# Optimization experiments

Measured on AMD Instinct MI355X. Metric: run time of the kernel, lower is better.

The kernel has to match this reference:

```python
import jax, jax.numpy as jnp
import numpy as np
from jax import lax

N = 5000          # num atoms
E = 4             # num edge types
DIM_H = 128
VOCAB = 100       # num_atoms_vocab; embedding table has VOCAB+1 rows
T = 4             # max_time_steps


def setup_inputs() -> dict:
    key = jax.random.key(0)
    k1, k2, k3, k4 = jax.random.split(key, 4)
    atom_arr = jax.random.randint(k1, (N,), 0, VOCAB, dtype=jnp.int64 if jax.config.read('jax_enable_x64') else jnp.int32)
    adjs = jax.random.randint(k2, (E, N, N), 0, 2, dtype=jnp.int32)
    # learned parameters
    embedding = jax.random.normal(k3, (VOCAB + 1, DIM_H), dtype=jnp.float32) * 0.05
    limit = float(np.sqrt(6.0 / (DIM_H + DIM_H)))  # glorot uniform
    H_edges = jax.random.uniform(k4, (E, DIM_H, DIM_H), minval=-limit, maxval=limit, dtype=jnp.float32)
    return {
        "atom_arr": atom_arr,
        "adjs": adjs,
        "max_time_steps": T,
        "embedding": embedding,
        "H_edges": H_edges,
    }


def reference(atom_arr, adjs, max_time_steps, embedding, H_edges):
    # h_v^0 = embedding lookup, [N, H]
    h0 = embedding[atom_arr]
    # adjacency mask as float, [E, N, N]
    A = (adjs == 1).astype(h0.dtype)

    def step(h, _):
        # original: for each node v, edge type e: H_e @ sum_{u: adj[e,v,u]==1} h_u
        agg = jnp.einsum('evu,uh->evh', A, h)          # neighbor sum per edge type
        msg = jnp.einsum('eij,evj->vi', H_edges, agg)  # edge-type transform + sum over e
        h_new = jax.nn.sigmoid(h + msg)
        return h_new, h_new

    _, h_all = lax.scan(step, h0, None, length=max_time_steps)
    return h_all  # [T, N, H]
```

## Files before the change

### kernel.cpp

```cpp
#include <hip/hip_runtime.h>

#define NROW 5000
#define NPAD 5120
#define KPAD 5120
#define KW   80
#define KC   80
#define KZ   4
#define KCQ  20
#define HDIM 128
#define FXS  4194304.0f
#define PART ((size_t)4 * NROW * HDIM)

typedef _Float16 f16x8 __attribute__((ext_vector_type(8)));
typedef float f32x16 __attribute__((ext_vector_type(16)));

__device__ __forceinline__ unsigned short f2h_int(int v) {
    union { _Float16 h; unsigned short u; } c;
    c.h = (_Float16)(float)v;
    return c.u;
}
__device__ __forceinline__ void fx_digits(float h, unsigned short& d1, unsigned short& d0) {
    int q = (int)rintf(h * FXS);
    d1 = f2h_int(q >> 11);
    d0 = f2h_int(q & 2047);
}

__device__ __forceinline__ size_t ht_idx(int pl, int kc, int i, int kin) {
    return (((size_t)pl * KC + kc) * HDIM + i) * 64 + kin;
}

__global__ __launch_bounds__(256) void prep_atom_kernel(const unsigned int* __restrict__ atomw,
                                                        int* __restrict__ atomIdx) {
    __shared__ int s_is64;
    if (threadIdx.x == 0) {
        bool all0 = true, anynz = false;
        for (int j = 0; j < 64; ++j) {
            unsigned lo = atomw[2 * j], hi = atomw[2 * j + 1];
            all0 = all0 && (hi == 0u);
            anynz = anynz || (lo != 0u);
        }
        s_is64 = (all0 && anynz) ? 1 : 0;
    }
    __syncthreads();
    int v = blockIdx.x * 256 + threadIdx.x;
    if (v < NROW) atomIdx[v] = s_is64 ? (int)atomw[2 * v] : (int)atomw[v];
}

__global__ __launch_bounds__(256) void prep_pack_kernel(const int* __restrict__ adjs,
                                                        unsigned long long* __restrict__ packed) {
    const int er = blockIdx.x;
    const int e = er / NPAD;
    const int r = er - e * NPAD;
    const int wave = threadIdx.x >> 6;
    const int lane = threadIdx.x & 63;
    const int* rowp = adjs + ((size_t)e * NROW + r) * NROW;
    unsigned long long* outp = packed + ((size_t)e * NPAD + r) * KW;
    const bool rok = (r < NROW);
    for (int c = wave; c < KW; c += 4) {
        int u = c * 64 + lane;
        int val = (rok && u < NROW) ? rowp[u] : 0;
        unsigned long long m = __ballot(val == 1);
        if (lane == 0) outp[c] = m;
    }
}

__global__ __launch_bounds__(256) void prep_h0T_kernel(const int* __restrict__ atomIdx,
                                                       const float* __restrict__ emb,
                                                       unsigned short* __restrict__ hTt) {
    const int i = blockIdx.y;
    const int v = blockIdx.x * 256 + threadIdx.x;
    float val = 0.f;
    if (v < NROW) val = emb[(size_t)atomIdx[v] * HDIM + i];
    unsigned short d1, d0;
    fx_digits(val, d1, d0);
    hTt[ht_idx(0, v >> 6, i, v & 63)] = d1;
    hTt[ht_idx(1, v >> 6, i, v & 63)] = d0;
}

__global__ __launch_bounds__(256) void prep_h0f_kernel(const int* __restrict__ atomIdx,
                                                       const float* __restrict__ emb,
                                                       float* __restrict__ h) {
    int idx = blockIdx.x * 256 + threadIdx.x;
    int v = idx >> 7, i = idx & 127;
    h[idx] = emb[(size_t)atomIdx[v] * HDIM + i];
}

__global__ __launch_bounds__(256) void prep_Ht_kernel(const float* __restrict__ H,
                                                      float* __restrict__ Htr) {
    int idx = blockIdx.x * 256 + threadIdx.x;
    int e = idx >> 14;
    int j = (idx >> 7) & 127;
    int i = idx & 127;
    Htr[idx] = H[((size_t)e * HDIM + i) * HDIM + j];
}

__global__ __launch_bounds__(256, 2) void gemm1_kernel(const uint2* __restrict__ packed2,
                                                       const unsigned short* __restrict__ hTt,
                                                       float* __restrict__ agg) {
    const int m0 = blockIdx.x * 128;
    const int e = blockIdx.y;
    const int kz = blockIdx.z;
    const int tid = threadIdx.x;
    const int lane = tid & 63;
    const int wave = tid >> 6;
    const int l31 = lane & 31;
    const int l1 = lane >> 5;
    const int sh2 = l1 * 8;
    const int cb = wave * 32;
    const int col = cb + l31;

    f32x16 acc[2][4];
#pragma unroll
    for (int pl = 0; pl < 2; ++pl)
#pragma unroll
        for (int mt = 0; mt < 4; ++mt) acc[pl][mt] = (f32x16)(0.f);

    const uint2* ap[4];
#pragma unroll
    for (int mt = 0; mt < 4; ++mt)
        ap[mt] = packed2 + ((size_t)e * NPAD + (m0 + mt * 32 + l31)) * KW;

    const _Float16* bbase = (const _Float16*)hTt;
    const int kc0 = kz * KCQ;
    const _Float16* bp[2];
#pragma unroll
    for (int pl = 0; pl < 2; ++pl)
        bp[pl] = bbase + (((size_t)pl * KC + kc0) * HDIM + col) * 64 + sh2;

    for (int kc = kc0; kc < kc0 + KCQ; ++kc) {
        uint2 aw[4];
#pragma unroll
        for (int mt = 0; mt < 4; ++mt) aw[mt] = ap[mt][kc];
        const size_t coff = (size_t)(kc - kc0) * (HDIM * 64);

        f16x8 bf[2][4];
#pragma unroll
        for (int pl = 0; pl < 2; ++pl)
#pragma unroll
            for (int kk = 0; kk < 4; ++kk)
                bf[pl][kk] = *(const f16x8*)(bp[pl] + coff + kk * 16);

#pragma unroll
        for (int kk = 0; kk < 4; ++kk) {
#pragma unroll
            for (int mt = 0; mt < 4; ++mt) {
                unsigned int w = (kk < 2) ? aw[mt].x : aw[mt].y;
                unsigned int b = (w >> ((kk & 1) * 16 + sh2)) & 0xFFu;
                unsigned int y = b | (b << 15);
                union { unsigned int u[4]; f16x8 h; } A;
#pragma unroll
                for (int q = 0; q < 4; ++q)
                    A.u[q] = ((y >> (2 * q)) & 0x00010001u) * 0x3C00u;
#pragma unroll
                for (int pl = 0; pl < 2; ++pl)
                    acc[pl][mt] = __builtin_amdgcn_mfma_f32_32x32x16_f16(
                        A.h, bf[pl][kk], acc[pl][mt], 0, 0, 0);
            }
        }
    }

    float* aggz = agg + (size_t)kz * PART;
#pragma unroll
    for (int mt = 0; mt < 4; ++mt)
#pragma unroll
        for (int reg = 0; reg < 16; ++reg) {
            int row = (reg & 3) + 8 * (reg >> 2) + 4 * l1;
            int v = m0 + mt * 32 + row;
            if (v < NROW) {
                double d = (double)acc[0][mt][reg] * 2048.0 + (double)acc[1][mt][reg];
                aggz[((size_t)e * NROW + v) * HDIM + col] = (float)(d * (1.0 / 4194304.0));
            }
        }
}

__global__ __launch_bounds__(256) void gemm2_kernel(const float* __restrict__ agg,
                                                    const float* __restrict__ Htr,
                                                    float* __restrict__ h,
                                                    float* __restrict__ outp,
                                                    unsigned short* __restrict__ hTt) {
    __shared__ float aggs[16][512];
    __shared__ unsigned short hs[2][128][16];
    const int v0 = blockIdx.x * 16;
    const int tid = threadIdx.x;

#pragma unroll
    for (int it = 0; it < 8; ++it) {
        int idx = it * 256 + tid;
        int vv = idx >> 7;
        int ej = (idx & 127) * 4;
        int e = ej >> 7, j = ej & 127;
        int v = v0 + vv;
        float4 val = make_float4(0.f, 0.f, 0.f, 0.f);
        if (v < NROW) {
            size_t o = ((size_t)e * NROW + v) * HDIM + j;
            float4 a0 = *(const float4*)&agg[o];
            float4 a1 = *(const float4*)&agg[PART + o];
            float4 a2 = *(const float4*)&agg[2 * PART + o];
            float4 a3 = *(const float4*)&agg[3 * PART + o];
            val = make_float4((a0.x + a1.x) + (a2.x + a3.x), (a0.y + a1.y) + (a2.y + a3.y),
                              (a0.z + a1.z) + (a2.z + a3.z), (a0.w + a1.w) + (a2.w + a3.w));
        }
        *(float4*)&aggs[vv][ej] = val;
    }
    __syncthreads();

    const int i = tid & 127;
    const int vg = tid >> 7;
    float m4[8][4];
#pragma unroll
    for (int vv = 0; vv < 8; ++vv)
#pragma unroll
        for (int k = 0; k < 4; ++k) m4[vv][k] = 0.f;

    for (int c = 0; c < 512; c += 4) {
        float w0 = Htr[(size_t)(c + 0) * HDIM + i];
        float w1 = Htr[(size_t)(c + 1) * HDIM + i];
        float w2 = Htr[(size_t)(c + 2) * HDIM + i];
        float w3 = Htr[(size_t)(c + 3) * HDIM + i];
#pragma unroll
        for (int vv = 0; vv < 8; ++vv) {
            const float4 a = *(const float4*)&aggs[vg * 8 + vv][c];
            m4[vv][0] += a.x * w0;
            m4[vv][1] += a.y * w1;
            m4[vv][2] += a.z * w2;
            m4[vv][3] += a.w * w3;
        }
    }

#pragma unroll
    for (int vv = 0; vv < 8; ++vv) {
        int v = v0 + vg * 8 + vv;
        unsigned short d1 = 0, d0 = 0;
        if (v < NROW) {
            size_t o = (size_t)v * HDIM + i;
            float msg = (m4[vv][0] + m4[vv][1]) + (m4[vv][2] + m4[vv][3]);
            float x = h[o] + msg;
            float s = 1.0f / (1.0f + expf(-x));
            outp[o] = s;
            h[o] = s;
            fx_digits(s, d1, d0);
        }
        hs[0][i][vg * 8 + vv] = d1;
        hs[1][i][vg * 8 + vv] = d0;
    }
    __syncthreads();
    if (tid < 128) {
#pragma unroll
        for (int pl = 0; pl < 2; ++pl) {
            uint4* d = (uint4*)&hTt[ht_idx(pl, v0 >> 6, tid, v0 & 63)];
            const uint4* sp = (const uint4*)&hs[pl][tid][0];
            d[0] = sp[0];
            d[1] = sp[1];
        }
    }
}

extern "C" void kernel_launch(void* const* d_in, const int* in_sizes, int n_in,
                              void* d_out, int out_size, void* d_ws, size_t ws_size,
                              hipStream_t stream) {
    const unsigned int* atomw = (const unsigned int*)d_in[0];
    const int* adjs = (const int*)d_in[1];
    const float* emb = (const float*)d_in[3];
    const float* H = (const float*)d_in[4];
    float* out = (float*)d_out;

    char* ws = (char*)d_ws;
    unsigned long long* packed = (unsigned long long*)ws;
    size_t off = (size_t)4 * NPAD * KW * 8;
    unsigned short* hTt = (unsigned short*)(ws + off);
    off += (size_t)2 * KC * HDIM * 64 * 2;
    float* hf = (float*)(ws + off);
    off += (size_t)NROW * HDIM * 4;
    float* agg = (float*)(ws + off);
    off += (size_t)KZ * PART * 4;
    float* Htr = (float*)(ws + off);
    off += (size_t)4 * HDIM * HDIM * 4;
    int* atomIdx = (int*)(ws + off);
    off += (size_t)NROW * 4;

    prep_atom_kernel<<<dim3((NROW + 255) / 256), 256, 0, stream>>>(atomw, atomIdx);
    prep_pack_kernel<<<dim3(4 * NPAD), 256, 0, stream>>>(adjs, packed);
    prep_h0T_kernel<<<dim3(KPAD / 256, HDIM), 256, 0, stream>>>(atomIdx, emb, hTt);
    prep_h0f_kernel<<<dim3(NROW * HDIM / 256), 256, 0, stream>>>(atomIdx, emb, hf);
    prep_Ht_kernel<<<dim3(4 * HDIM * HDIM / 256), 256, 0, stream>>>(H, Htr);

    for (int t = 0; t < 4; ++t) {
        gemm1_kernel<<<dim3(NPAD / 128, 4, KZ), 256, 0, stream>>>((const uint2*)packed, hTt, agg);
        gemm2_kernel<<<dim3((NROW + 15) / 16), 256, 0, stream>>>(agg, Htr, hf,
                                                                 out + (size_t)t * NROW * HDIM, hTt);
    }
}
```

Before: 1.098 ms.

## Transpose packed adjacency and reorder h tiles for coalesced gemm1 loads, enlarge M tile

Stores the packed adjacency bitmasks column-major (chunk-major across rows), so lanes in a wave read consecutive 64-bit words. It also relayouts the fixed-point fp16 h operand so each MFMA B fragment is a contiguous 16-byte load per lane. In addition, the per-block M tile grows from 4 to 5 MFMA row tiles (160 rows), which reuses each B fragment across more rows. The larger tile raises accumulator register pressure, and the grid shrinks to 32x4x4 blocks, which may hurt occupancy and wave balance.

```diff
diff --git a/kernel.cpp b/kernel.cpp
--- a/kernel.cpp
+++ b/kernel.cpp
@@ -8,6 +8,8 @@
 #define KZ   4
 #define KCQ  20
 #define HDIM 128
+#define MTI  5
+#define MROWS (MTI * 32)
 #define FXS  4194304.0f
 #define PART ((size_t)4 * NROW * HDIM)
 
@@ -25,8 +27,8 @@
     d0 = f2h_int(q & 2047);
 }
 
-__device__ __forceinline__ size_t ht_idx(int pl, int kc, int i, int kin) {
-    return (((size_t)pl * KC + kc) * HDIM + i) * 64 + kin;
+__device__ __forceinline__ size_t bt_idx(int kc, int pl, int kk, int half, int col, int j) {
+    return (((((size_t)kc * 2 + pl) * 4 + kk) * 2 + half) * 128 + col) * 8 + j;
 }
 
 __global__ __launch_bounds__(256) void prep_atom_kernel(const unsigned int* __restrict__ atomw,
@@ -47,20 +49,20 @@
 }
 
 __global__ __launch_bounds__(256) void prep_pack_kernel(const int* __restrict__ adjs,
-                                                        unsigned long long* __restrict__ packed) {
+                                                        unsigned long long* __restrict__ packedT) {
     const int er = blockIdx.x;
     const int e = er / NPAD;
     const int r = er - e * NPAD;
     const int wave = threadIdx.x >> 6;
     const int lane = threadIdx.x & 63;
     const int* rowp = adjs + ((size_t)e * NROW + r) * NROW;
-    unsigned long long* outp = packed + ((size_t)e * NPAD + r) * KW;
+    unsigned long long* outp = packedT + (size_t)e * KC * NPAD + r;
     const bool rok = (r < NROW);
     for (int c = wave; c < KW; c += 4) {
         int u = c * 64 + lane;
         int val = (rok && u < NROW) ? rowp[u] : 0;
         unsigned long long m = __ballot(val == 1);
-        if (lane == 0) outp[c] = m;
+        if (lane == 0) outp[(size_t)c * NPAD] = m;
     }
 }
 
@@ -73,8 +75,9 @@
     if (v < NROW) val = emb[(size_t)atomIdx[v] * HDIM + i];
     unsigned short d1, d0;
     fx_digits(val, d1, d0);
-    hTt[ht_idx(0, v >> 6, i, v & 63)] = d1;
-    hTt[ht_idx(1, v >> 6, i, v & 63)] = d0;
+    const int kc = v >> 6, kk = (v >> 4) & 3, half = (v >> 3) & 1, j = v & 7;
+    hTt[bt_idx(kc, 0, kk, half, i, j)] = d1;
+    hTt[bt_idx(kc, 1, kk, half, i, j)] = d0;
 }
 
 __global__ __launch_bounds__(256) void prep_h0f_kernel(const int* __restrict__ atomIdx,
@@ -94,10 +97,10 @@
     Htr[idx] = H[((size_t)e * HDIM + i) * HDIM + j];
 }
 
-__global__ __launch_bounds__(256, 2) void gemm1_kernel(const uint2* __restrict__ packed2,
+__global__ __launch_bounds__(256, 2) void gemm1_kernel(const unsigned long long* __restrict__ packedT,
                                                        const unsigned short* __restrict__ hTt,
                                                        float* __restrict__ agg) {
-    const int m0 = blockIdx.x * 128;
+    const int m0 = blockIdx.x * MROWS;
     const int e = blockIdx.y;
     const int kz = blockIdx.z;
     const int tid = threadIdx.x;
@@ -106,45 +109,38 @@
     const int l31 = lane & 31;
     const int l1 = lane >> 5;
     const int sh2 = l1 * 8;
-    const int cb = wave * 32;
-    const int col = cb + l31;
-
-    f32x16 acc[2][4];
+    const int col = wave * 32 + l31;
+
+    f32x16 acc[2][MTI];
 #pragma unroll
     for (int pl = 0; pl < 2; ++pl)
 #pragma unroll
-        for (int mt = 0; mt < 4; ++mt) acc[pl][mt] = (f32x16)(0.f);
-
-    const uint2* ap[4];
-#pragma unroll
-    for (int mt = 0; mt < 4; ++mt)
-        ap[mt] = packed2 + ((size_t)e * NPAD + (m0 + mt * 32 + l31)) * KW;
-
-    const _Float16* bbase = (const _Float16*)hTt;
+        for (int mt = 0; mt < MTI; ++mt) acc[pl][mt] = (f32x16)(0.f);
+
     const int kc0 = kz * KCQ;
-    const _Float16* bp[2];
-#pragma unroll
-    for (int pl = 0; pl < 2; ++pl)
-        bp[pl] = bbase + (((size_t)pl * KC + kc0) * HDIM + col) * 64 + sh2;
-
-    for (int kc = kc0; kc < kc0 + KCQ; ++kc) {
-        uint2 aw[4];
-#pragma unroll
-        for (int mt = 0; mt < 4; ++mt) aw[mt] = ap[mt][kc];
-        const size_t coff = (size_t)(kc - kc0) * (HDIM * 64);
+    const unsigned long long* ap = packedT + ((size_t)e * KC + kc0) * NPAD + m0 + l31;
+    const _Float16* bp = (const _Float16*)hTt + (size_t)kc0 * 16384 + (size_t)l1 * 1024 + (size_t)col * 8;
+
+    for (int kc = 0; kc < KCQ; ++kc) {
+        unsigned long long aw[MTI];
+#pragma unroll
+        for (int mt = 0; mt < MTI; ++mt) aw[mt] = ap[mt * 32];
 
         f16x8 bf[2][4];
 #pragma unroll
         for (int pl = 0; pl < 2; ++pl)
 #pragma unroll
             for (int kk = 0; kk < 4; ++kk)
-                bf[pl][kk] = *(const f16x8*)(bp[pl] + coff + kk * 16);
+                bf[pl][kk] = *(const f16x8*)(bp + pl * 8192 + kk * 2048);
+
+        ap += NPAD;
+        bp += 16384;
 
 #pragma unroll
         for (int kk = 0; kk < 4; ++kk) {
 #pragma unroll
-            for (int mt = 0; mt < 4; ++mt) {
-                unsigned int w = (kk < 2) ? aw[mt].x : aw[mt].y;
+            for (int mt = 0; mt < MTI; ++mt) {
+                unsigned int w = (kk < 2) ? (unsigned int)aw[mt] : (unsigned int)(aw[mt] >> 32);
                 unsigned int b = (w >> ((kk & 1) * 16 + sh2)) & 0xFFu;
                 unsigned int y = b | (b << 15);
                 union { unsigned int u[4]; f16x8 h; } A;
@@ -161,7 +157,7 @@
 
     float* aggz = agg + (size_t)kz * PART;
 #pragma unroll
-    for (int mt = 0; mt < 4; ++mt)
+    for (int mt = 0; mt < MTI; ++mt)
 #pragma unroll
         for (int reg = 0; reg < 16; ++reg) {
             int row = (reg & 3) + 8 * (reg >> 2) + 4 * l1;
@@ -245,12 +241,12 @@
     }
     __syncthreads();
     if (tid < 128) {
+        const int kc = v0 >> 6, kk = (v0 >> 4) & 3;
 #pragma unroll
         for (int pl = 0; pl < 2; ++pl) {
-            uint4* d = (uint4*)&hTt[ht_idx(pl, v0 >> 6, tid, v0 & 63)];
             const uint4* sp = (const uint4*)&hs[pl][tid][0];
-            d[0] = sp[0];
-            d[1] = sp[1];
+            *(uint4*)&hTt[bt_idx(kc, pl, kk, 0, tid, 0)] = sp[0];
+            *(uint4*)&hTt[bt_idx(kc, pl, kk, 1, tid, 0)] = sp[1];
         }
     }
 }
@@ -265,8 +261,8 @@
     float* out = (float*)d_out;
 
     char* ws = (char*)d_ws;
-    unsigned long long* packed = (unsigned long long*)ws;
-    size_t off = (size_t)4 * NPAD * KW * 8;
+    unsigned long long* packedT = (unsigned long long*)ws;
+    size_t off = (size_t)4 * KC * NPAD * 8;
     unsigned short* hTt = (unsigned short*)(ws + off);
     off += (size_t)2 * KC * HDIM * 64 * 2;
     float* hf = (float*)(ws + off);
@@ -279,13 +275,13 @@
     off += (size_t)NROW * 4;
 
     prep_atom_kernel<<<dim3((NROW + 255) / 256), 256, 0, stream>>>(atomw, atomIdx);
-    prep_pack_kernel<<<dim3(4 * NPAD), 256, 0, stream>>>(adjs, packed);
+    prep_pack_kernel<<<dim3(4 * NPAD), 256, 0, stream>>>(adjs, packedT);
     prep_h0T_kernel<<<dim3(KPAD / 256, HDIM), 256, 0, stream>>>(atomIdx, emb, hTt);
     prep_h0f_kernel<<<dim3(NROW * HDIM / 256), 256, 0, stream>>>(atomIdx, emb, hf);
     prep_Ht_kernel<<<dim3(4 * HDIM * HDIM / 256), 256, 0, stream>>>(H, Htr);
 
     for (int t = 0; t < 4; ++t) {
-        gemm1_kernel<<<dim3(NPAD / 128, 4, KZ), 256, 0, stream>>>((const uint2*)packed, hTt, agg);
+        gemm1_kernel<<<dim3(NPAD / MROWS, 4, KZ), 256, 0, stream>>>(packedT, hTt, agg);
         gemm2_kernel<<<dim3((NROW + 15) / 16), 256, 0, stream>>>(agg, Htr, hf,
                                                                  out + (size_t)t * NROW * HDIM, hTt);
     }
```

Result: faster. 1.057 ms (-3.7%).
